# Kernel optimization log

Measured on AMD Instinct MI355X. Metric: run time of the kernel, lower is better.

## Reference

```python
import jax, jax.numpy as jnp
import numpy as np

D = 1024      # features
C = 768       # context dim
H = 16        # heads
HD = D // H   # head dim = 64
N = 2048      # query tokens
M = 2048      # context tokens
EPS = 1e-12
SCALE = float(np.sqrt(HD))


def layernorm(x, w, b):
    c = x - x.mean(axis=-1, keepdims=True)
    s = (c * c).mean(axis=-1, keepdims=True)
    return c * jax.lax.rsqrt(s + EPS) * w + b


def setup_inputs() -> dict:
    key = jax.random.key(0)
    ks = jax.random.split(key, 10)
    sc = 0.02
    return {
        "x": jax.random.normal(ks[0], (N, D), jnp.float32),
        "ctx": jax.random.normal(ks[1], (M, C), jnp.float32),
        # attention projections (Projection: normal*0.02, zero bias)
        "wq": jax.random.normal(ks[2], (D, D), jnp.float32) * sc,
        "bq": jnp.zeros((D,), jnp.float32),
        "wk": jax.random.normal(ks[3], (C, D), jnp.float32) * sc,
        "bk": jnp.zeros((D,), jnp.float32),
        "wv": jax.random.normal(ks[4], (C, D), jnp.float32) * sc,
        "bv": jnp.zeros((D,), jnp.float32),
        "wo": jax.random.normal(ks[5], (D, D), jnp.float32) * sc,
        "bo": jnp.zeros((D,), jnp.float32),
        # MLP
        "w1": jax.random.normal(ks[6], (D, 4 * D), jnp.float32) * sc,
        "b1": jnp.zeros((4 * D,), jnp.float32),
        "w2": jax.random.normal(ks[7], (4 * D, D), jnp.float32) * sc,
        "b2": jnp.zeros((D,), jnp.float32),
        # layernorms
        "qn_w": jnp.ones((D,), jnp.float32), "qn_b": jnp.zeros((D,), jnp.float32),
        "kvn_w": jnp.ones((C,), jnp.float32), "kvn_b": jnp.zeros((C,), jnp.float32),
        "pn_w": jnp.ones((D,), jnp.float32), "pn_b": jnp.zeros((D,), jnp.float32),
    }


def reference(x, ctx, wq, bq, wk, bk, wv, bv, wo, bo, w1, b1, w2, b2,
              qn_w, qn_b, kvn_w, kvn_b, pn_w, pn_b):
    # pre-norm cross-attention
    xq = layernorm(x, qn_w, qn_b)          # [n, d]
    kv = layernorm(ctx, kvn_w, kvn_b)      # [m, c]
    q = (xq @ wq + bq).reshape(N, H, HD).transpose(1, 0, 2)   # [h, n, hd]
    k = (kv @ wk + bk).reshape(M, H, HD).transpose(1, 0, 2)   # [h, m, hd]
    v = (kv @ wv + bv).reshape(M, H, HD).transpose(1, 0, 2)   # [h, m, hd]
    attn = jax.nn.softmax(jnp.einsum('hnd,hmd->hnm', q, k) / SCALE, axis=-1)
    o = jnp.einsum('hnm,hmd->hnd', attn, v).transpose(1, 0, 2).reshape(N, D)
    x = (o @ wo + bo) + x
    # MLP block
    h = layernorm(x, pn_w, pn_b)
    h = jax.nn.gelu(h @ w1 + b1) @ w2 + b2
    return h + x
```

## Files before the change

kernel.cpp:

```cpp
#include <hip/hip_runtime.h>

typedef __bf16 bf16;
typedef __bf16 bf16x4 __attribute__((ext_vector_type(4)));
typedef __bf16 bf16x8 __attribute__((ext_vector_type(8)));
typedef float f32x4 __attribute__((ext_vector_type(4)));

#define N_TOK 2048
#define M_TOK 2048
#define DIM 1024
#define CDIM 768
#define DFF 4096

static __device__ __forceinline__ void async16(const void* g, void* l) {
  __builtin_amdgcn_global_load_lds((const __attribute__((address_space(1))) void*)g,
                                   (__attribute__((address_space(3))) void*)l, 16, 0, 0);
}

struct ConvArgs {
  const void* src[12];
  bf16* dst[12];
  int n[12];
  const void* xprobe;
};
__global__ __launch_bounds__(256) void conv_small_kernel(ConvArgs a, int* flag) {
  __shared__ int cnt;
  if (threadIdx.x == 0) cnt = 0;
  __syncthreads();
  const unsigned* w = (const unsigned*)a.xprobe;
  int ok = 0;
  for (int i = threadIdx.x; i < 512; i += 256) {
    unsigned lo = w[i] & 0xFFFFu;
    float f = __uint_as_float(lo << 16);
    if (lo == 0u || (fabsf(f) > 1e-3f && fabsf(f) < 1e3f)) ok++;
  }
  atomicAdd(&cnt, ok);
  __syncthreads();
  const bool isbf = (cnt >= 256);
  if (blockIdx.x == 0 && threadIdx.x == 0) *flag = isbf ? 1 : 0;
  const int b = blockIdx.x;
  const void* in = a.src[b];
  bf16* out = a.dst[b];
  const int n = a.n[b];
  for (int i = threadIdx.x; i < n; i += 256)
    out[i] = isbf ? ((const bf16*)in)[i] : (bf16)((const float*)in)[i];
}

struct TmArgs {
  const void* src[4];
  bf16* dst[4];
  int r0[4], Rcnt[4], c0[4], Cfull[4], gx[4], gy[4];
  int force_bf;
};
__global__ __launch_bounds__(256) void tmulti_kernel(TmArgs a, const int* flag) {
  const int z = blockIdx.z;
  if ((int)blockIdx.x >= a.gx[z] || (int)blockIdx.y >= a.gy[z]) return;
  __shared__ bf16 t[32][33];
  const bool isbf = a.force_bf || (*flag != 0);
  const void* in = a.src[z];
  bf16* out = a.dst[z];
  const int Rcnt = a.Rcnt[z], Cfull = a.Cfull[z];
  const int cb = blockIdx.x * 32, rb = blockIdx.y * 32;
  const int tx = threadIdx.x & 31, ty = threadIdx.x >> 5;
#pragma unroll
  for (int i = 0; i < 4; i++) {
    const size_t r = (size_t)(a.r0[z] + rb + ty + i * 8);
    const size_t c = (size_t)(a.c0[z] + cb + tx);
    float v = isbf ? (float)((const bf16*)in)[r * Cfull + c]
                   : ((const float*)in)[r * Cfull + c];
    t[ty + i * 8][tx] = (bf16)v;
  }
  __syncthreads();
#pragma unroll
  for (int i = 0; i < 4; i++)
    out[(size_t)(cb + ty + i * 8) * Rcnt + rb + tx] = t[tx][ty + i * 8];
}

__global__ __launch_bounds__(256) void ln_pair_kernel(
    const void* __restrict__ x0, const bf16* w0, const bf16* b0, bf16* o0,
    const void* __restrict__ x1, const bf16* w1, const bf16* b1, bf16* o1,
    const int* flag) {
  const bool isbf = (*flag != 0);
  const int cols = (blockIdx.y == 0) ? DIM : CDIM;
  const void* x = (blockIdx.y == 0) ? x0 : x1;
  const bf16* w = (blockIdx.y == 0) ? w0 : w1;
  const bf16* b = (blockIdx.y == 0) ? b0 : b1;
  bf16* outp = (blockIdx.y == 0) ? o0 : o1;
  const int row = blockIdx.x;
  const bf16* xr_b = (const bf16*)x + (size_t)row * cols;
  const float* xr_f = (const float*)x + (size_t)row * cols;
  bf16* orow = outp + (size_t)row * cols;
  float s = 0.f, ss = 0.f;
  for (int c = threadIdx.x; c < cols; c += 256) {
    float v = isbf ? (float)xr_b[c] : xr_f[c];
    s += v; ss += v * v;
  }
  for (int d = 1; d < 64; d <<= 1) { s += __shfl_xor(s, d, 64); ss += __shfl_xor(ss, d, 64); }
  __shared__ float sh[8];
  const int wv = threadIdx.x >> 6, lane = threadIdx.x & 63;
  if (lane == 0) { sh[wv] = s; sh[4 + wv] = ss; }
  __syncthreads();
  s = sh[0] + sh[1] + sh[2] + sh[3];
  ss = sh[4] + sh[5] + sh[6] + sh[7];
  const float mean = s / cols;
  float var = ss / cols - mean * mean;
  var = fmaxf(var, 0.f);
  const float r = rsqrtf(var + 1e-12f);
  for (int c = threadIdx.x; c < cols; c += 256) {
    float v = isbf ? (float)xr_b[c] : xr_f[c];
    orow[c] = (bf16)((v - mean) * r * (float)w[c] + (float)b[c]);
  }
}

__global__ __launch_bounds__(256) void ln_kernel(
    const bf16* __restrict__ x, const bf16* __restrict__ w, const bf16* __restrict__ b,
    bf16* __restrict__ out, int cols) {
  const int row = blockIdx.x;
  const bf16* xr = x + (size_t)row * cols;
  bf16* orow = out + (size_t)row * cols;
  float s = 0.f, ss = 0.f;
  for (int c = threadIdx.x; c < cols; c += 256) {
    float v = (float)xr[c];
    s += v; ss += v * v;
  }
  for (int d = 1; d < 64; d <<= 1) { s += __shfl_xor(s, d, 64); ss += __shfl_xor(ss, d, 64); }
  __shared__ float sh[8];
  const int wv = threadIdx.x >> 6, lane = threadIdx.x & 63;
  if (lane == 0) { sh[wv] = s; sh[4 + wv] = ss; }
  __syncthreads();
  s = sh[0] + sh[1] + sh[2] + sh[3];
  ss = sh[4] + sh[5] + sh[6] + sh[7];
  const float mean = s / cols;
  float var = ss / cols - mean * mean;
  var = fmaxf(var, 0.f);
  const float r = rsqrtf(var + 1e-12f);
  for (int c = threadIdx.x; c < cols; c += 256) {
    float v = (float)xr[c];
    orow[c] = (bf16)((v - mean) * r * (float)w[c] + (float)b[c]);
  }
}

__device__ __forceinline__ float gelu_f(float x) {
  float u = 0.7978845608028654f * (x + 0.044715f * x * x * x);
  return 0.5f * x * (1.f + tanhf(u));
}

template <int EPI>
__global__ __launch_bounds__(256) void gemm64db(
    const bf16* __restrict__ A, const bf16* __restrict__ Bt,
    const bf16* __restrict__ bias, const void* __restrict__ resid,
    void* __restrict__ Cout, int K, int ldc, const int* flag) {
  __shared__ __align__(16) bf16 As[2][64 * 64];
  __shared__ __align__(16) bf16 Bs[2][64 * 64];
  const int tid = threadIdx.x;
  const int lane = tid & 63, wv = tid >> 6;
  const int lq = lane >> 4, lm = lane & 15;
  const int row0 = blockIdx.y * 64, col0 = blockIdx.x * 64;
  const int wr = (wv >> 1) * 32, wc = (wv & 1) * 32;

  const int sr = lane >> 3;
  const int sc = ((lane & 7) ^ sr) * 8;
  const int swz = (lm & 7) << 3;

  f32x4 acc[2][2] = {};

  const bf16* Abase = A + (size_t)(row0 + wv * 16 + sr) * K + sc;
  const bf16* Bbase = Bt + (size_t)(col0 + wv * 16 + sr) * K + sc;

  const int nt = K >> 6;
#pragma unroll
  for (int b = 0; b < 2; b++) {
    async16(Abase + (size_t)(b * 8) * K, &As[0][wv * 1024 + b * 512]);
    async16(Bbase + (size_t)(b * 8) * K, &Bs[0][wv * 1024 + b * 512]);
  }
  __syncthreads();

  int cur = 0;
  for (int t = 0; t < nt; ++t) {
    if (t + 1 < nt) {
      const int k1 = (t + 1) << 6;
#pragma unroll
      for (int b = 0; b < 2; b++) {
        async16(Abase + (size_t)(b * 8) * K + k1, &As[cur ^ 1][wv * 1024 + b * 512]);
        async16(Bbase + (size_t)(b * 8) * K + k1, &Bs[cur ^ 1][wv * 1024 + b * 512]);
      }
    }
#pragma unroll
    for (int kh = 0; kh < 2; kh++) {
      const int cofs = (kh * 32 + lq * 8) ^ swz;
      bf16x8 af[2], bfv[2];
#pragma unroll
      for (int i = 0; i < 2; i++)
        af[i] = *(const bf16x8*)&As[cur][(wr + i * 16 + lm) * 64 + cofs];
#pragma unroll
      for (int j = 0; j < 2; j++)
        bfv[j] = *(const bf16x8*)&Bs[cur][(wc + j * 16 + lm) * 64 + cofs];
#pragma unroll
      for (int i = 0; i < 2; i++)
#pragma unroll
        for (int j = 0; j < 2; j++)
          acc[i][j] = __builtin_amdgcn_mfma_f32_16x16x32_bf16(af[i], bfv[j], acc[i][j], 0, 0, 0);
    }
    __syncthreads();
    cur ^= 1;
  }

  const bool isbf = (*flag != 0);
#pragma unroll
  for (int i = 0; i < 2; i++) {
    const int rb = row0 + wr + i * 16 + lq * 4;
#pragma unroll
    for (int j = 0; j < 2; j++) {
      const int c = col0 + wc + j * 16 + lm;
      const float bv = (EPI != 5) ? (float)bias[c] : 0.f;
#pragma unroll
      for (int rg = 0; rg < 4; rg++) {
        const size_t idx = (size_t)(rb + rg) * ldc + c;
        float v = acc[i][j][rg] + bv;
        if (EPI == 1)
          v += isbf ? (float)((const bf16*)resid)[idx] : ((const float*)resid)[idx];
        if (EPI == 2) v = gelu_f(v);
        if (EPI == 4) v += (float)((const bf16*)resid)[idx];
        if (EPI == 5)
          v += isbf ? (float)((bf16*)Cout)[idx] : ((float*)Cout)[idx];
        if (EPI == 4 || EPI == 5) {
          if (isbf) ((bf16*)Cout)[idx] = (bf16)v;
          else      ((float*)Cout)[idx] = v;
        } else {
          ((bf16*)Cout)[idx] = (bf16)v;
        }
      }
    }
  }
}

struct QkvArgs {
  const bf16* A[3];
  const bf16* Bt[3];
  const bf16* bias[3];
  bf16* C[3];
  int K[3], ldc[3], gx[3], gy[3], brow[3];
};
__global__ __launch_bounds__(256) void gemm64db_qkv(QkvArgs a) {
  const int z = blockIdx.z;
  if ((int)blockIdx.x >= a.gx[z] || (int)blockIdx.y >= a.gy[z]) return;
  const bf16* A = a.A[z];
  const bf16* Bt = a.Bt[z];
  const int K = a.K[z];
  __shared__ __align__(16) bf16 As[2][64 * 64];
  __shared__ __align__(16) bf16 Bs[2][64 * 64];
  const int tid = threadIdx.x;
  const int lane = tid & 63, wv = tid >> 6;
  const int lq = lane >> 4, lm = lane & 15;
  const int row0 = blockIdx.y * 64, col0 = blockIdx.x * 64;
  const int wr = (wv >> 1) * 32, wc = (wv & 1) * 32;

  const int sr = lane >> 3;
  const int sc = ((lane & 7) ^ sr) * 8;
  const int swz = (lm & 7) << 3;

  f32x4 acc[2][2] = {};

  const bf16* Abase = A + (size_t)(row0 + wv * 16 + sr) * K + sc;
  const bf16* Bbase = Bt + (size_t)(col0 + wv * 16 + sr) * K + sc;

  const int nt = K >> 6;
#pragma unroll
  for (int b = 0; b < 2; b++) {
    async16(Abase + (size_t)(b * 8) * K, &As[0][wv * 1024 + b * 512]);
    async16(Bbase + (size_t)(b * 8) * K, &Bs[0][wv * 1024 + b * 512]);
  }
  __syncthreads();

  int cur = 0;
  for (int t = 0; t < nt; ++t) {
    if (t + 1 < nt) {
      const int k1 = (t + 1) << 6;
#pragma unroll
      for (int b = 0; b < 2; b++) {
        async16(Abase + (size_t)(b * 8) * K + k1, &As[cur ^ 1][wv * 1024 + b * 512]);
        async16(Bbase + (size_t)(b * 8) * K + k1, &Bs[cur ^ 1][wv * 1024 + b * 512]);
      }
    }
#pragma unroll
    for (int kh = 0; kh < 2; kh++) {
      const int cofs = (kh * 32 + lq * 8) ^ swz;
      bf16x8 af[2], bfv[2];
#pragma unroll
      for (int i = 0; i < 2; i++)
        af[i] = *(const bf16x8*)&As[cur][(wr + i * 16 + lm) * 64 + cofs];
#pragma unroll
      for (int j = 0; j < 2; j++)
        bfv[j] = *(const bf16x8*)&Bs[cur][(wc + j * 16 + lm) * 64 + cofs];
#pragma unroll
      for (int i = 0; i < 2; i++)
#pragma unroll
        for (int j = 0; j < 2; j++)
          acc[i][j] = __builtin_amdgcn_mfma_f32_16x16x32_bf16(af[i], bfv[j], acc[i][j], 0, 0, 0);
    }
    __syncthreads();
    cur ^= 1;
  }

  const bf16* bias = a.bias[z];
  bf16* C = a.C[z];
  const int ldc = a.ldc[z];
  const bool brow = a.brow[z] != 0;
#pragma unroll
  for (int i = 0; i < 2; i++) {
    const int rb = row0 + wr + i * 16 + lq * 4;
#pragma unroll
    for (int j = 0; j < 2; j++) {
      const int c = col0 + wc + j * 16 + lm;
      const float bcol = brow ? 0.f : (float)bias[c];
#pragma unroll
      for (int rg = 0; rg < 4; rg++) {
        const float bv = brow ? (float)bias[rb + rg] : bcol;
        C[(size_t)(rb + rg) * ldc + c] = (bf16)(acc[i][j][rg] + bv);
      }
    }
  }
}

__global__ __launch_bounds__(256) void attn_kernel(
    const bf16* __restrict__ q, const bf16* __restrict__ k,
    const bf16* __restrict__ vT, bf16* __restrict__ pO0, bf16* __restrict__ pO1,
    float* __restrict__ l0, float* __restrict__ l1) {
  __shared__ __align__(16) bf16 KPs[128 * 64];
  __shared__ __align__(16) bf16 Vs[64 * 128];
  const int tid = threadIdx.x, lane = tid & 63, wv = tid >> 6;
  const int lq = lane >> 4, lm = lane & 15;
  const int fid = blockIdx.x + 32 * (blockIdx.y + 16 * blockIdx.z);
  const int sid = (fid & 7) * 128 + (fid >> 3);
  const int n0 = (sid & 31) * 64;
  const int h = (sid >> 5) & 15;
  const int half = sid >> 9;
  const int mbeg = half * (M_TOK / 2), mend = mbeg + M_TOK / 2;
  bf16* pO = half ? pO1 : pO0;
  float* lb = half ? l1 : l0;

  bf16x8 qf[2];
#pragma unroll
  for (int f = 0; f < 2; f++)
    qf[f] = *(const bf16x8*)&q[(size_t)(n0 + wv * 16 + lm) * DIM + h * 64 + f * 32 + lq * 8];

  f32x4 oacc[4] = {};
  float lsum = 0.f;
  const float sc = 0.125f * 1.4426950408889634f;

  bf16x8 kreg[4], vreg[4];
#pragma unroll
  for (int it = 0; it < 4; it++) {
    const int e = tid * 8 + it * 2048;
    kreg[it] = *(const bf16x8*)&k[(size_t)(mbeg + (e >> 6)) * DIM + h * 64 + (e & 63)];
    vreg[it] = *(const bf16x8*)&vT[(size_t)(h * 64 + (e >> 7)) * M_TOK + mbeg + (e & 127)];
  }

  for (int m0 = mbeg; m0 < mend; m0 += 128) {
    asm volatile("s_waitcnt lgkmcnt(0)" ::: "memory");
    __builtin_amdgcn_s_barrier();
#pragma unroll
    for (int it = 0; it < 4; it++) {
      const int e = tid * 8 + it * 2048;
      const int kr = e >> 6, kc = e & 63;
      *(bf16x8*)&KPs[kr * 64 + (kc ^ ((kr & 7) << 3))] = kreg[it];
      const int vr = e >> 7, vc = e & 127;
      *(bf16x8*)&Vs[vr * 128 + (vc ^ ((vr & 7) << 3))] = vreg[it];
    }
    if (m0 + 128 < mend) {
      const int m1 = m0 + 128;
#pragma unroll
      for (int it = 0; it < 4; it++) {
        const int e = tid * 8 + it * 2048;
        kreg[it] = *(const bf16x8*)&k[(size_t)(m1 + (e >> 6)) * DIM + h * 64 + (e & 63)];
        vreg[it] = *(const bf16x8*)&vT[(size_t)(h * 64 + (e >> 7)) * M_TOK + m1 + (e & 127)];
      }
    }
    asm volatile("s_waitcnt lgkmcnt(0)" ::: "memory");
    __builtin_amdgcn_s_barrier();

    f32x4 s[8];
#pragma unroll
    for (int j = 0; j < 8; j++) {
      const int kswz = (lm & 7) << 3;
      bf16x8 kf0 = *(const bf16x8*)&KPs[(j * 16 + lm) * 64 + ((lq * 8) ^ kswz)];
      bf16x8 kf1 = *(const bf16x8*)&KPs[(j * 16 + lm) * 64 + ((32 + lq * 8) ^ kswz)];
      f32x4 z = {};
      z = __builtin_amdgcn_mfma_f32_16x16x32_bf16(kf0, qf[0], z, 0, 0, 0);
      s[j] = __builtin_amdgcn_mfma_f32_16x16x32_bf16(kf1, qf[1], z, 0, 0, 0);
    }
    asm volatile("s_waitcnt lgkmcnt(0)" ::: "memory");
    __builtin_amdgcn_s_barrier();

#pragma unroll
    for (int j = 0; j < 8; j++) {
      bf16x4 pw;
#pragma unroll
      for (int rg = 0; rg < 4; rg++) {
        const float pv = exp2f(s[j][rg] * sc);
        lsum += pv;
        pw[rg] = (bf16)pv;
      }
      *(bf16x4*)&KPs[(wv * 16 + lm) * 128 + ((j * 16 + lq * 4) ^ ((lm & 7) << 3))] = pw;
    }

#pragma unroll
    for (int kk = 0; kk < 4; kk++) {
      bf16x8 pf = *(const bf16x8*)&KPs[(wv * 16 + lm) * 128 +
                                       ((kk * 32 + lq * 8) ^ ((lm & 7) << 3))];
#pragma unroll
      for (int dt = 0; dt < 4; dt++) {
        bf16x8 vf = *(const bf16x8*)&Vs[(dt * 16 + lm) * 128 +
                                        ((kk * 32 + lq * 8) ^ ((lm & 7) << 3))];
        oacc[dt] = __builtin_amdgcn_mfma_f32_16x16x32_bf16(vf, pf, oacc[dt], 0, 0, 0);
      }
    }
  }

  lsum += __shfl_xor(lsum, 16, 64);
  lsum += __shfl_xor(lsum, 32, 64);
  if (lane < 16) lb[h * N_TOK + n0 + wv * 16 + lane] = lsum;

  const int rn = n0 + wv * 16 + lm;
#pragma unroll
  for (int dt = 0; dt < 4; dt++) {
    bf16x4 ow;
#pragma unroll
    for (int rg = 0; rg < 4; rg++) ow[rg] = (bf16)oacc[dt][rg];
    *(bf16x4*)&pO[(size_t)rn * DIM + h * 64 + dt * 16 + lq * 4] = ow;
  }
}

__global__ __launch_bounds__(256) void attn_combine(
    const bf16* __restrict__ pO0, const bf16* __restrict__ pO1,
    const float* __restrict__ l0, const float* __restrict__ l1,
    bf16* __restrict__ om) {
  const int i4 = (blockIdx.x * 256 + threadIdx.x) * 4;
  const int n = i4 >> 10;
  const int h = (i4 & 1023) >> 6;
  const float rinv = 1.f / (l0[h * N_TOK + n] + l1[h * N_TOK + n]);
  bf16x4 a = *(const bf16x4*)&pO0[i4];
  bf16x4 b = *(const bf16x4*)&pO1[i4];
  bf16x4 o;
#pragma unroll
  for (int r = 0; r < 4; r++) o[r] = (bf16)(((float)a[r] + (float)b[r]) * rinv);
  *(bf16x4*)&om[i4] = o;
}

extern "C" void kernel_launch(void* const* d_in, const int* in_sizes, int n_in,
                              void* d_out, int out_size, void* d_ws, size_t ws_size,
                              hipStream_t stream) {
  const void* x_r     = d_in[0];
  const void* ctx_r   = d_in[1];
  const void* wq_r    = d_in[2];
  const void* bq_r    = d_in[3];
  const void* wk_r    = d_in[4];
  const void* bk_r    = d_in[5];
  const void* wv_r    = d_in[6];
  const void* bv_r    = d_in[7];
  const void* wo_r    = d_in[8];
  const void* bo_r    = d_in[9];
  const void* w1_r    = d_in[10];
  const void* b1_r    = d_in[11];
  const void* w2_r    = d_in[12];
  const void* b2_r    = d_in[13];
  const void* qnw_r   = d_in[14];
  const void* qnb_r   = d_in[15];
  const void* kvnw_r  = d_in[16];
  const void* kvnb_r  = d_in[17];
  const void* pnw_r   = d_in[18];
  const void* pnb_r   = d_in[19];

  bf16* p = (bf16*)d_ws;
  const size_t MEG = 1024 * 1024;
  bf16* qm  = p;             bf16* hln = qm;
  bf16* km  = p + 2 * MEG;   bf16* xat = km;
  bf16* wC  = p + 4 * MEG;
  bf16* xq  = p + 8 * MEG;   bf16* pO0 = xq;   bf16* om = xq;
  bf16* vTb = p + 10 * MEG;
  bf16* kvn = p + 12 * MEG;  bf16* pO1 = kvn;
  bf16* h1h = p + 10 * MEG;
  bf16* SM  = p + 14 * MEG;
  int* flag = (int*)(p + 14 * MEG + 16384);

  bf16* wqT = wC;
  bf16* wkT = wC + 1 * MEG;
  bf16* wvT = wC + 1 * MEG + 786432;
  bf16* woT = wC + 2 * MEG + 524288;
  bf16* w1Th = wC;
  bf16* w2Th = wC + 2 * MEG;
  float* l0 = (float*)wC;
  float* l1 = l0 + N_TOK * 16;

  bf16* bqc = SM, *bkc = SM + 1024, *bvc = SM + 2048, *boc = SM + 3072;
  bf16* b1c = SM + 4096, *b2c = SM + 8192;
  bf16* qnw = SM + 9216, *qnb = SM + 10240;
  bf16* kvnw = SM + 11264, *kvnb = SM + 12032;
  bf16* pnw = SM + 12800, *pnb = SM + 13824;

  ConvArgs ca;
  ca.src[0] = bq_r;   ca.dst[0] = bqc;  ca.n[0] = DIM;
  ca.src[1] = bk_r;   ca.dst[1] = bkc;  ca.n[1] = DIM;
  ca.src[2] = bv_r;   ca.dst[2] = bvc;  ca.n[2] = DIM;
  ca.src[3] = bo_r;   ca.dst[3] = boc;  ca.n[3] = DIM;
  ca.src[4] = b1_r;   ca.dst[4] = b1c;  ca.n[4] = DFF;
  ca.src[5] = b2_r;   ca.dst[5] = b2c;  ca.n[5] = DIM;
  ca.src[6] = qnw_r;  ca.dst[6] = qnw;  ca.n[6] = DIM;
  ca.src[7] = qnb_r;  ca.dst[7] = qnb;  ca.n[7] = DIM;
  ca.src[8] = kvnw_r; ca.dst[8] = kvnw; ca.n[8] = CDIM;
  ca.src[9] = kvnb_r; ca.dst[9] = kvnb; ca.n[9] = CDIM;
  ca.src[10] = pnw_r; ca.dst[10] = pnw; ca.n[10] = DIM;
  ca.src[11] = pnb_r; ca.dst[11] = pnb; ca.n[11] = DIM;
  ca.xprobe = x_r;
  conv_small_kernel<<<12, 256, 0, stream>>>(ca, flag);

  ln_pair_kernel<<<dim3(2048, 2), 256, 0, stream>>>(x_r, qnw, qnb, xq,
                                                    ctx_r, kvnw, kvnb, kvn, flag);

  {
    TmArgs ta;
    ta.force_bf = 0;
    ta.src[0] = wq_r; ta.dst[0] = wqT; ta.r0[0] = 0; ta.Rcnt[0] = DIM;
    ta.c0[0] = 0; ta.Cfull[0] = DIM; ta.gx[0] = 32; ta.gy[0] = 32;
    ta.src[1] = wk_r; ta.dst[1] = wkT; ta.r0[1] = 0; ta.Rcnt[1] = CDIM;
    ta.c0[1] = 0; ta.Cfull[1] = DIM; ta.gx[1] = 32; ta.gy[1] = 24;
    ta.src[2] = wv_r; ta.dst[2] = wvT; ta.r0[2] = 0; ta.Rcnt[2] = CDIM;
    ta.c0[2] = 0; ta.Cfull[2] = DIM; ta.gx[2] = 32; ta.gy[2] = 24;
    ta.src[3] = wo_r; ta.dst[3] = woT; ta.r0[3] = 0; ta.Rcnt[3] = DIM;
    ta.c0[3] = 0; ta.Cfull[3] = DIM; ta.gx[3] = 32; ta.gy[3] = 32;
    tmulti_kernel<<<dim3(32, 32, 4), 256, 0, stream>>>(ta, flag);
  }

  {
    QkvArgs qa;
    qa.A[0] = xq;  qa.Bt[0] = wqT; qa.bias[0] = bqc; qa.C[0] = qm;
    qa.K[0] = DIM;  qa.ldc[0] = DIM;   qa.gx[0] = 16; qa.gy[0] = 32; qa.brow[0] = 0;
    qa.A[1] = kvn; qa.Bt[1] = wkT; qa.bias[1] = bkc; qa.C[1] = km;
    qa.K[1] = CDIM; qa.ldc[1] = DIM;   qa.gx[1] = 16; qa.gy[1] = 32; qa.brow[1] = 0;
    qa.A[2] = wvT; qa.Bt[2] = kvn; qa.bias[2] = bvc; qa.C[2] = vTb;
    qa.K[2] = CDIM; qa.ldc[2] = M_TOK; qa.gx[2] = 32; qa.gy[2] = 16; qa.brow[2] = 1;
    gemm64db_qkv<<<dim3(32, 32, 3), 256, 0, stream>>>(qa);
  }

  attn_kernel<<<dim3(32, 16, 2), 256, 0, stream>>>(qm, km, vTb, pO0, pO1, l0, l1);
  attn_combine<<<2048, 256, 0, stream>>>(pO0, pO1, l0, l1, om);

  gemm64db<1><<<dim3(16, 32), 256, 0, stream>>>(om, woT, boc, x_r, xat, DIM, DIM, flag);

  ln_kernel<<<N_TOK, 256, 0, stream>>>(xat, pnw, pnb, hln, DIM);

  for (int hh = 0; hh < 2; hh++) {
    TmArgs ta;
    ta.force_bf = 0;
    ta.src[0] = w1_r; ta.dst[0] = w1Th; ta.r0[0] = 0; ta.Rcnt[0] = DIM;
    ta.c0[0] = hh * 2048; ta.Cfull[0] = DFF; ta.gx[0] = 64; ta.gy[0] = 32;
    ta.src[1] = w2_r; ta.dst[1] = w2Th; ta.r0[1] = hh * 2048; ta.Rcnt[1] = 2048;
    ta.c0[1] = 0; ta.Cfull[1] = DIM; ta.gx[1] = 32; ta.gy[1] = 64;
    ta.src[2] = ta.src[0]; ta.dst[2] = ta.dst[0]; ta.r0[2] = 0; ta.Rcnt[2] = 32;
    ta.c0[2] = 0; ta.Cfull[2] = DIM; ta.gx[2] = 0; ta.gy[2] = 0;
    ta.src[3] = ta.src[0]; ta.dst[3] = ta.dst[0]; ta.r0[3] = 0; ta.Rcnt[3] = 32;
    ta.c0[3] = 0; ta.Cfull[3] = DIM; ta.gx[3] = 0; ta.gy[3] = 0;
    tmulti_kernel<<<dim3(64, 64, 2), 256, 0, stream>>>(ta, flag);

    gemm64db<2><<<dim3(32, 32), 256, 0, stream>>>(hln, w1Th, b1c + hh * 2048, nullptr,
                                                  h1h, DIM, 2048, flag);
    if (hh == 0)
      gemm64db<4><<<dim3(16, 32), 256, 0, stream>>>(h1h, w2Th, b2c, xat, d_out,
                                                    2048, DIM, flag);
    else
      gemm64db<5><<<dim3(16, 32), 256, 0, stream>>>(h1h, w2Th, b2c, nullptr, d_out,
                                                    2048, DIM, flag);
  }
}
```

Measured before the change: 352.7 us.

## Fuse prep kernels, merge post-attention LN with MLP weight transposes, add MFMA priority hints

Merges the bias/weight conversion, the four attention weight transposes and both input layernorms into one prep kernel. It also fuses the post-attention layernorm with the first-half w1/w2 transposes into a post kernel. This cuts launch count and serialization between small kernels. The QKV GEMM grid is tightened to drop idle blocks, with a swapped block order for the Q/K parts. The attention MFMA loops gain s_setprio hints. The layernorms now cache the row in shared memory and read raw weights, at the cost of more shared memory per block and more complex multi-role kernels.

```diff
diff --git a/kernel.cpp b/kernel.cpp
--- a/kernel.cpp
+++ b/kernel.cpp
@@ -16,86 +16,54 @@
                                    (__attribute__((address_space(3))) void*)l, 16, 0, 0);
 }
 
-struct ConvArgs {
-  const void* src[12];
-  bf16* dst[12];
-  int n[12];
-  const void* xprobe;
-};
-__global__ __launch_bounds__(256) void conv_small_kernel(ConvArgs a, int* flag) {
-  __shared__ int cnt;
-  if (threadIdx.x == 0) cnt = 0;
+__device__ __forceinline__ bool detect_bf(const void* xprobe, float* sbuf) {
+  int* cnt = (int*)sbuf;
+  if (threadIdx.x == 0) *cnt = 0;
   __syncthreads();
-  const unsigned* w = (const unsigned*)a.xprobe;
+  const unsigned* w = (const unsigned*)xprobe;
   int ok = 0;
   for (int i = threadIdx.x; i < 512; i += 256) {
     unsigned lo = w[i] & 0xFFFFu;
     float f = __uint_as_float(lo << 16);
     if (lo == 0u || (fabsf(f) > 1e-3f && fabsf(f) < 1e3f)) ok++;
   }
-  atomicAdd(&cnt, ok);
+  atomicAdd(cnt, ok);
   __syncthreads();
-  const bool isbf = (cnt >= 256);
-  if (blockIdx.x == 0 && threadIdx.x == 0) *flag = isbf ? 1 : 0;
-  const int b = blockIdx.x;
-  const void* in = a.src[b];
-  bf16* out = a.dst[b];
-  const int n = a.n[b];
-  for (int i = threadIdx.x; i < n; i += 256)
-    out[i] = isbf ? ((const bf16*)in)[i] : (bf16)((const float*)in)[i];
-}
-
-struct TmArgs {
-  const void* src[4];
-  bf16* dst[4];
-  int r0[4], Rcnt[4], c0[4], Cfull[4], gx[4], gy[4];
-  int force_bf;
-};
-__global__ __launch_bounds__(256) void tmulti_kernel(TmArgs a, const int* flag) {
-  const int z = blockIdx.z;
-  if ((int)blockIdx.x >= a.gx[z] || (int)blockIdx.y >= a.gy[z]) return;
-  __shared__ bf16 t[32][33];
-  const bool isbf = a.force_bf || (*flag != 0);
-  const void* in = a.src[z];
-  bf16* out = a.dst[z];
-  const int Rcnt = a.Rcnt[z], Cfull = a.Cfull[z];
+  return *cnt >= 256;
+}
+
+__device__ __forceinline__ void t32(const void* in, bf16* out, int r0, int Rcnt,
+                                    int c0, int Cfull, bool isbf, bf16* t) {
   const int cb = blockIdx.x * 32, rb = blockIdx.y * 32;
   const int tx = threadIdx.x & 31, ty = threadIdx.x >> 5;
 #pragma unroll
   for (int i = 0; i < 4; i++) {
-    const size_t r = (size_t)(a.r0[z] + rb + ty + i * 8);
-    const size_t c = (size_t)(a.c0[z] + cb + tx);
+    const size_t r = (size_t)(r0 + rb + ty + i * 8);
+    const size_t c = (size_t)(c0 + cb + tx);
     float v = isbf ? (float)((const bf16*)in)[r * Cfull + c]
                    : ((const float*)in)[r * Cfull + c];
-    t[ty + i * 8][tx] = (bf16)v;
+    t[(ty + i * 8) * 33 + tx] = (bf16)v;
   }
   __syncthreads();
 #pragma unroll
   for (int i = 0; i < 4; i++)
-    out[(size_t)(cb + ty + i * 8) * Rcnt + rb + tx] = t[tx][ty + i * 8];
-}
-
-__global__ __launch_bounds__(256) void ln_pair_kernel(
-    const void* __restrict__ x0, const bf16* w0, const bf16* b0, bf16* o0,
-    const void* __restrict__ x1, const bf16* w1, const bf16* b1, bf16* o1,
-    const int* flag) {
-  const bool isbf = (*flag != 0);
-  const int cols = (blockIdx.y == 0) ? DIM : CDIM;
-  const void* x = (blockIdx.y == 0) ? x0 : x1;
-  const bf16* w = (blockIdx.y == 0) ? w0 : w1;
-  const bf16* b = (blockIdx.y == 0) ? b0 : b1;
-  bf16* outp = (blockIdx.y == 0) ? o0 : o1;
-  const int row = blockIdx.x;
+    out[(size_t)(cb + ty + i * 8) * Rcnt + rb + tx] = t[tx * 33 + ty + i * 8];
+}
+
+__device__ __forceinline__ void ln_row(const void* x, const void* wr, const void* br,
+                                       bf16* outp, int cols, int row,
+                                       bool in_bf, bool w_bf,
+                                       float* xrow, float* sh) {
   const bf16* xr_b = (const bf16*)x + (size_t)row * cols;
   const float* xr_f = (const float*)x + (size_t)row * cols;
   bf16* orow = outp + (size_t)row * cols;
   float s = 0.f, ss = 0.f;
   for (int c = threadIdx.x; c < cols; c += 256) {
-    float v = isbf ? (float)xr_b[c] : xr_f[c];
+    float v = in_bf ? (float)xr_b[c] : xr_f[c];
+    xrow[c] = v;
     s += v; ss += v * v;
   }
   for (int d = 1; d < 64; d <<= 1) { s += __shfl_xor(s, d, 64); ss += __shfl_xor(ss, d, 64); }
-  __shared__ float sh[8];
   const int wv = threadIdx.x >> 6, lane = threadIdx.x & 63;
   if (lane == 0) { sh[wv] = s; sh[4 + wv] = ss; }
   __syncthreads();
@@ -106,37 +74,76 @@
   var = fmaxf(var, 0.f);
   const float r = rsqrtf(var + 1e-12f);
   for (int c = threadIdx.x; c < cols; c += 256) {
-    float v = isbf ? (float)xr_b[c] : xr_f[c];
-    orow[c] = (bf16)((v - mean) * r * (float)w[c] + (float)b[c]);
-  }
-}
-
-__global__ __launch_bounds__(256) void ln_kernel(
-    const bf16* __restrict__ x, const bf16* __restrict__ w, const bf16* __restrict__ b,
-    bf16* __restrict__ out, int cols) {
-  const int row = blockIdx.x;
-  const bf16* xr = x + (size_t)row * cols;
-  bf16* orow = out + (size_t)row * cols;
-  float s = 0.f, ss = 0.f;
-  for (int c = threadIdx.x; c < cols; c += 256) {
-    float v = (float)xr[c];
-    s += v; ss += v * v;
-  }
-  for (int d = 1; d < 64; d <<= 1) { s += __shfl_xor(s, d, 64); ss += __shfl_xor(ss, d, 64); }
-  __shared__ float sh[8];
-  const int wv = threadIdx.x >> 6, lane = threadIdx.x & 63;
-  if (lane == 0) { sh[wv] = s; sh[4 + wv] = ss; }
-  __syncthreads();
-  s = sh[0] + sh[1] + sh[2] + sh[3];
-  ss = sh[4] + sh[5] + sh[6] + sh[7];
-  const float mean = s / cols;
-  float var = ss / cols - mean * mean;
-  var = fmaxf(var, 0.f);
-  const float r = rsqrtf(var + 1e-12f);
-  for (int c = threadIdx.x; c < cols; c += 256) {
-    float v = (float)xr[c];
-    orow[c] = (bf16)((v - mean) * r * (float)w[c] + (float)b[c]);
-  }
+    const float wv2 = w_bf ? (float)((const bf16*)wr)[c] : ((const float*)wr)[c];
+    const float bv2 = w_bf ? (float)((const bf16*)br)[c] : ((const float*)br)[c];
+    orow[c] = (bf16)((xrow[c] - mean) * r * wv2 + bv2);
+  }
+}
+
+struct PrepArgs {
+  const void* tsrc[4]; bf16* tdst[4]; int tRcnt[4], tCfull[4], tgy[4];
+  const void* x; const void* qnw; const void* qnb; bf16* xq;
+  const void* ctx; const void* kvnw; const void* kvnb; bf16* kvn;
+  const void* csrc[12]; bf16* cdst[12]; int cn[12];
+  const void* xprobe;
+};
+__global__ __launch_bounds__(256) void prep_kernel(PrepArgs a, int* flag) {
+  __shared__ __align__(16) float sbuf[1040];
+  const int z = blockIdx.z;
+  const bool isbf = detect_bf(a.xprobe, sbuf);
+  if (z < 4) {
+    if ((int)blockIdx.y >= a.tgy[z]) return;
+    t32(a.tsrc[z], a.tdst[z], 0, a.tRcnt[z], 0, a.tCfull[z], isbf, (bf16*)sbuf);
+  } else if (z < 8) {
+    const int row = blockIdx.x + 32 * blockIdx.y + (z & 1) * 1024;
+    if (z < 6) ln_row(a.x,   a.qnw,  a.qnb,  a.xq,  DIM,  row, isbf, isbf, sbuf, sbuf + 1024);
+    else       ln_row(a.ctx, a.kvnw, a.kvnb, a.kvn, CDIM, row, isbf, isbf, sbuf, sbuf + 1024);
+  } else {
+    const int b = blockIdx.x + 32 * blockIdx.y;
+    if (b == 0 && threadIdx.x == 0) *flag = isbf ? 1 : 0;
+    if (b >= 12) return;
+    const void* in = a.csrc[b];
+    bf16* out = a.cdst[b];
+    const int n = a.cn[b];
+    for (int i = threadIdx.x; i < n; i += 256)
+      out[i] = isbf ? ((const bf16*)in)[i] : (bf16)((const float*)in)[i];
+  }
+}
+
+struct PostArgs {
+  const void* w1; bf16* w1T;
+  const void* w2; bf16* w2T;
+  const bf16* xat; const void* pnw; const void* pnb; bf16* hln;
+};
+__global__ __launch_bounds__(256) void post_kernel(PostArgs a, const int* flag) {
+  __shared__ __align__(16) float sbuf[1040];
+  const int z = blockIdx.z;
+  const bool isbf = (*flag != 0);
+  if (z == 0) {
+    if (blockIdx.y >= 32) return;
+    t32(a.w1, a.w1T, 0, DIM, 0, DFF, isbf, (bf16*)sbuf);
+  } else if (z == 1) {
+    if (blockIdx.x >= 32) return;
+    t32(a.w2, a.w2T, 0, 2048, 0, DIM, isbf, (bf16*)sbuf);
+  } else {
+    const int row = blockIdx.x + 64 * blockIdx.y;
+    if (row >= N_TOK) return;
+    ln_row(a.xat, a.pnw, a.pnb, a.hln, DIM, row, true, isbf, sbuf, sbuf + 1024);
+  }
+}
+
+struct TmArgs {
+  const void* src[4];
+  bf16* dst[4];
+  int r0[4], Rcnt[4], c0[4], Cfull[4], gx[4], gy[4];
+  int force_bf;
+};
+__global__ __launch_bounds__(256) void tmulti_kernel(TmArgs a, const int* flag) {
+  const int z = blockIdx.z;
+  if ((int)blockIdx.x >= a.gx[z] || (int)blockIdx.y >= a.gy[z]) return;
+  __shared__ bf16 t[32 * 33];
+  const bool isbf = a.force_bf || (*flag != 0);
+  t32(a.src[z], a.dst[z], a.r0[z], a.Rcnt[z], a.c0[z], a.Cfull[z], isbf, t);
 }
 
 __device__ __forceinline__ float gelu_f(float x) {
@@ -238,11 +245,13 @@
   const bf16* Bt[3];
   const bf16* bias[3];
   bf16* C[3];
-  int K[3], ldc[3], gx[3], gy[3], brow[3];
+  int K[3], ldc[3], brow[3];
 };
 __global__ __launch_bounds__(256) void gemm64db_qkv(QkvArgs a) {
   const int z = blockIdx.z;
-  if ((int)blockIdx.x >= a.gx[z] || (int)blockIdx.y >= a.gy[z]) return;
+  int bx, by;
+  if (z < 2) { bx = blockIdx.y; by = blockIdx.x; }
+  else       { bx = blockIdx.x; by = blockIdx.y; }
   const bf16* A = a.A[z];
   const bf16* Bt = a.Bt[z];
   const int K = a.K[z];
@@ -251,7 +260,7 @@
   const int tid = threadIdx.x;
   const int lane = tid & 63, wv = tid >> 6;
   const int lq = lane >> 4, lm = lane & 15;
-  const int row0 = blockIdx.y * 64, col0 = blockIdx.x * 64;
+  const int row0 = by * 64, col0 = bx * 64;
   const int wr = (wv >> 1) * 32, wc = (wv & 1) * 32;
 
   const int sr = lane >> 3;
@@ -379,6 +388,7 @@
     __builtin_amdgcn_s_barrier();
 
     f32x4 s[8];
+    __builtin_amdgcn_s_setprio(1);
 #pragma unroll
     for (int j = 0; j < 8; j++) {
       const int kswz = (lm & 7) << 3;
@@ -388,6 +398,7 @@
       z = __builtin_amdgcn_mfma_f32_16x16x32_bf16(kf0, qf[0], z, 0, 0, 0);
       s[j] = __builtin_amdgcn_mfma_f32_16x16x32_bf16(kf1, qf[1], z, 0, 0, 0);
     }
+    __builtin_amdgcn_s_setprio(0);
     asm volatile("s_waitcnt lgkmcnt(0)" ::: "memory");
     __builtin_amdgcn_s_barrier();
 
@@ -403,6 +414,7 @@
       *(bf16x4*)&KPs[(wv * 16 + lm) * 128 + ((j * 16 + lq * 4) ^ ((lm & 7) << 3))] = pw;
     }
 
+    __builtin_amdgcn_s_setprio(1);
 #pragma unroll
     for (int kk = 0; kk < 4; kk++) {
       bf16x8 pf = *(const bf16x8*)&KPs[(wv * 16 + lm) * 128 +
@@ -414,6 +426,7 @@
         oacc[dt] = __builtin_amdgcn_mfma_f32_16x16x32_bf16(vf, pf, oacc[dt], 0, 0, 0);
       }
     }
+    __builtin_amdgcn_s_setprio(0);
   }
 
   lsum += __shfl_xor(lsum, 16, 64);
@@ -497,77 +510,74 @@
   bf16* kvnw = SM + 11264, *kvnb = SM + 12032;
   bf16* pnw = SM + 12800, *pnb = SM + 13824;
 
-  ConvArgs ca;
-  ca.src[0] = bq_r;   ca.dst[0] = bqc;  ca.n[0] = DIM;
-  ca.src[1] = bk_r;   ca.dst[1] = bkc;  ca.n[1] = DIM;
-  ca.src[2] = bv_r;   ca.dst[2] = bvc;  ca.n[2] = DIM;
-  ca.src[3] = bo_r;   ca.dst[3] = boc;  ca.n[3] = DIM;
-  ca.src[4] = b1_r;   ca.dst[4] = b1c;  ca.n[4] = DFF;
-  ca.src[5] = b2_r;   ca.dst[5] = b2c;  ca.n[5] = DIM;
-  ca.src[6] = qnw_r;  ca.dst[6] = qnw;  ca.n[6] = DIM;
-  ca.src[7] = qnb_r;  ca.dst[7] = qnb;  ca.n[7] = DIM;
-  ca.src[8] = kvnw_r; ca.dst[8] = kvnw; ca.n[8] = CDIM;
-  ca.src[9] = kvnb_r; ca.dst[9] = kvnb; ca.n[9] = CDIM;
-  ca.src[10] = pnw_r; ca.dst[10] = pnw; ca.n[10] = DIM;
-  ca.src[11] = pnb_r; ca.dst[11] = pnb; ca.n[11] = DIM;
-  ca.xprobe = x_r;
-  conv_small_kernel<<<12, 256, 0, stream>>>(ca, flag);
-
-  ln_pair_kernel<<<dim3(2048, 2), 256, 0, stream>>>(x_r, qnw, qnb, xq,
-                                                    ctx_r, kvnw, kvnb, kvn, flag);
+  {
+    PrepArgs pa;
+    pa.tsrc[0] = wq_r; pa.tdst[0] = wqT; pa.tRcnt[0] = DIM;  pa.tCfull[0] = DIM; pa.tgy[0] = 32;
+    pa.tsrc[1] = wk_r; pa.tdst[1] = wkT; pa.tRcnt[1] = CDIM; pa.tCfull[1] = DIM; pa.tgy[1] = 24;
+    pa.tsrc[2] = wv_r; pa.tdst[2] = wvT; pa.tRcnt[2] = CDIM; pa.tCfull[2] = DIM; pa.tgy[2] = 24;
+    pa.tsrc[3] = wo_r; pa.tdst[3] = woT; pa.tRcnt[3] = DIM;  pa.tCfull[3] = DIM; pa.tgy[3] = 32;
+    pa.x = x_r;   pa.qnw = qnw_r;   pa.qnb = qnb_r;   pa.xq = xq;
+    pa.ctx = ctx_r; pa.kvnw = kvnw_r; pa.kvnb = kvnb_r; pa.kvn = kvn;
+    pa.csrc[0] = bq_r;   pa.cdst[0] = bqc;  pa.cn[0] = DIM;
+    pa.csrc[1] = bk_r;   pa.cdst[1] = bkc;  pa.cn[1] = DIM;
+    pa.csrc[2] = bv_r;   pa.cdst[2] = bvc;  pa.cn[2] = DIM;
+    pa.csrc[3] = bo_r;   pa.cdst[3] = boc;  pa.cn[3] = DIM;
+    pa.csrc[4] = b1_r;   pa.cdst[4] = b1c;  pa.cn[4] = DFF;
+    pa.csrc[5] = b2_r;   pa.cdst[5] = b2c;  pa.cn[5] = DIM;
+    pa.csrc[6] = qnw_r;  pa.cdst[6] = qnw;  pa.cn[6] = DIM;
+    pa.csrc[7] = qnb_r;  pa.cdst[7] = qnb;  pa.cn[7] = DIM;
+    pa.csrc[8] = kvnw_r; pa.cdst[8] = kvnw; pa.cn[8] = CDIM;
+    pa.csrc[9] = kvnb_r; pa.cdst[9] = kvnb; pa.cn[9] = CDIM;
+    pa.csrc[10] = pnw_r; pa.cdst[10] = pnw; pa.cn[10] = DIM;
+    pa.csrc[11] = pnb_r; pa.cdst[11] = pnb; pa.cn[11] = DIM;
+    pa.xprobe = x_r;
+    prep_kernel<<<dim3(32, 32, 9), 256, 0, stream>>>(pa, flag);
+  }
+
+  {
+    QkvArgs qa;
+    qa.A[0] = xq;  qa.Bt[0] = wqT; qa.bias[0] = bqc; qa.C[0] = qm;
+    qa.K[0] = DIM;  qa.ldc[0] = DIM;   qa.brow[0] = 0;
+    qa.A[1] = kvn; qa.Bt[1] = wkT; qa.bias[1] = bkc; qa.C[1] = km;
+    qa.K[1] = CDIM; qa.ldc[1] = DIM;   qa.brow[1] = 0;
+    qa.A[2] = wvT; qa.Bt[2] = kvn; qa.bias[2] = bvc; qa.C[2] = vTb;
+    qa.K[2] = CDIM; qa.ldc[2] = M_TOK; qa.brow[2] = 1;
+    gemm64db_qkv<<<dim3(32, 16, 3), 256, 0, stream>>>(qa);
+  }
+
+  attn_kernel<<<dim3(32, 16, 2), 256, 0, stream>>>(qm, km, vTb, pO0, pO1, l0, l1);
+  attn_combine<<<2048, 256, 0, stream>>>(pO0, pO1, l0, l1, om);
+
+  gemm64db<1><<<dim3(16, 32), 256, 0, stream>>>(om, woT, boc, x_r, xat, DIM, DIM, flag);
+
+  {
+    PostArgs po;
+    po.w1 = w1_r; po.w1T = w1Th;
+    po.w2 = w2_r; po.w2T = w2Th;
+    po.xat = xat; po.pnw = pnw_r; po.pnb = pnb_r; po.hln = hln;
+    post_kernel<<<dim3(64, 64, 3), 256, 0, stream>>>(po, flag);
+  }
+
+  gemm64db<2><<<dim3(32, 32), 256, 0, stream>>>(hln, w1Th, b1c, nullptr,
+                                                h1h, DIM, 2048, flag);
+  gemm64db<4><<<dim3(16, 32), 256, 0, stream>>>(h1h, w2Th, b2c, xat, d_out,
+                                                2048, DIM, flag);
 
   {
     TmArgs ta;
     ta.force_bf = 0;
-    ta.src[0] = wq_r; ta.dst[0] = wqT; ta.r0[0] = 0; ta.Rcnt[0] = DIM;
-    ta.c0[0] = 0; ta.Cfull[0] = DIM; ta.gx[0] = 32; ta.gy[0] = 32;
-    ta.src[1] = wk_r; ta.dst[1] = wkT; ta.r0[1] = 0; ta.Rcnt[1] = CDIM;
-    ta.c0[1] = 0; ta.Cfull[1] = DIM; ta.gx[1] = 32; ta.gy[1] = 24;
-    ta.src[2] = wv_r; ta.dst[2] = wvT; ta.r0[2] = 0; ta.Rcnt[2] = CDIM;
-    ta.c0[2] = 0; ta.Cfull[2] = DIM; ta.gx[2] = 32; ta.gy[2] = 24;
-    ta.src[3] = wo_r; ta.dst[3] = woT; ta.r0[3] = 0; ta.Rcnt[3] = DIM;
-    ta.c0[3] = 0; ta.Cfull[3] = DIM; ta.gx[3] = 32; ta.gy[3] = 32;
-    tmulti_kernel<<<dim3(32, 32, 4), 256, 0, stream>>>(ta, flag);
-  }
-
-  {
-    QkvArgs qa;
-    qa.A[0] = xq;  qa.Bt[0] = wqT; qa.bias[0] = bqc; qa.C[0] = qm;
-    qa.K[0] = DIM;  qa.ldc[0] = DIM;   qa.gx[0] = 16; qa.gy[0] = 32; qa.brow[0] = 0;
-    qa.A[1] = kvn; qa.Bt[1] = wkT; qa.bias[1] = bkc; qa.C[1] = km;
-    qa.K[1] = CDIM; qa.ldc[1] = DIM;   qa.gx[1] = 16; qa.gy[1] = 32; qa.brow[1] = 0;
-    qa.A[2] = wvT; qa.Bt[2] = kvn; qa.bias[2] = bvc; qa.C[2] = vTb;
-    qa.K[2] = CDIM; qa.ldc[2] = M_TOK; qa.gx[2] = 32; qa.gy[2] = 16; qa.brow[2] = 1;
-    gemm64db_qkv<<<dim3(32, 32, 3), 256, 0, stream>>>(qa);
-  }
-
-  attn_kernel<<<dim3(32, 16, 2), 256, 0, stream>>>(qm, km, vTb, pO0, pO1, l0, l1);
-  attn_combine<<<2048, 256, 0, stream>>>(pO0, pO1, l0, l1, om);
-
-  gemm64db<1><<<dim3(16, 32), 256, 0, stream>>>(om, woT, boc, x_r, xat, DIM, DIM, flag);
-
-  ln_kernel<<<N_TOK, 256, 0, stream>>>(xat, pnw, pnb, hln, DIM);
-
-  for (int hh = 0; hh < 2; hh++) {
-    TmArgs ta;
-    ta.force_bf = 0;
     ta.src[0] = w1_r; ta.dst[0] = w1Th; ta.r0[0] = 0; ta.Rcnt[0] = DIM;
-    ta.c0[0] = hh * 2048; ta.Cfull[0] = DFF; ta.gx[0] = 64; ta.gy[0] = 32;
-    ta.src[1] = w2_r; ta.dst[1] = w2Th; ta.r0[1] = hh * 2048; ta.Rcnt[1] = 2048;
+    ta.c0[0] = 2048; ta.Cfull[0] = DFF; ta.gx[0] = 64; ta.gy[0] = 32;
+    ta.src[1] = w2_r; ta.dst[1] = w2Th; ta.r0[1] = 2048; ta.Rcnt[1] = 2048;
     ta.c0[1] = 0; ta.Cfull[1] = DIM; ta.gx[1] = 32; ta.gy[1] = 64;
     ta.src[2] = ta.src[0]; ta.dst[2] = ta.dst[0]; ta.r0[2] = 0; ta.Rcnt[2] = 32;
     ta.c0[2] = 0; ta.Cfull[2] = DIM; ta.gx[2] = 0; ta.gy[2] = 0;
     ta.src[3] = ta.src[0]; ta.dst[3] = ta.dst[0]; ta.r0[3] = 0; ta.Rcnt[3] = 32;
     ta.c0[3] = 0; ta.Cfull[3] = DIM; ta.gx[3] = 0; ta.gy[3] = 0;
     tmulti_kernel<<<dim3(64, 64, 2), 256, 0, stream>>>(ta, flag);
-
-    gemm64db<2><<<dim3(32, 32), 256, 0, stream>>>(hln, w1Th, b1c + hh * 2048, nullptr,
-                                                  h1h, DIM, 2048, flag);
-    if (hh == 0)
-      gemm64db<4><<<dim3(16, 32), 256, 0, stream>>>(h1h, w2Th, b2c, xat, d_out,
-                                                    2048, DIM, flag);
-    else
-      gemm64db<5><<<dim3(16, 32), 256, 0, stream>>>(h1h, w2Th, b2c, nullptr, d_out,
-                                                    2048, DIM, flag);
-  }
-}
+  }
+  gemm64db<2><<<dim3(32, 32), 256, 0, stream>>>(hln, w1Th, b1c + 2048, nullptr,
+                                                h1h, DIM, 2048, flag);
+  gemm64db<5><<<dim3(16, 32), 256, 0, stream>>>(h1h, w2Th, b2c, nullptr, d_out,
+                                                2048, DIM, flag);
+}
```

Measured after the change: 347.1 us. Within noise of the previous version (-1.6%).
